# Optimization experiments

Measured on AMD Instinct MI355X. Metric: run time of the kernel, lower is better.

Reference implementation:

```python
import jax, jax.numpy as jnp
import numpy as np

N = 50000      # nodes
E = 800000     # edges (avg degree 16)
IN = 128       # in_channels
HID = 64       # hidden_channels
OUT = 64       # out_channels
H = 2          # attention heads
EDIM = 16      # edge feature dim
NEG_SLOPE = 0.2


def setup_inputs() -> dict:
    key = jax.random.key(0)
    ks = jax.random.split(key, 16)
    p = lambda k, shape: (jax.random.normal(k, shape, jnp.float32) * 0.1)
    return {
        'x': jax.random.normal(ks[0], (N, IN), jnp.float32),
        'edge_index': jax.random.randint(ks[1], (2, E), 0, N, dtype=jnp.int64),
        'edge_attr': jax.random.normal(ks[2], (E, EDIM), jnp.float32),
        # GAT layer 1 (in=IN -> HID, heads=H, concat=False, edge_dim=EDIM)
        'W1': p(ks[3], (IN, H * HID)),
        'We1': p(ks[4], (EDIM, H * HID)),
        'as1': p(ks[5], (H, HID)),
        'ad1': p(ks[6], (H, HID)),
        'ae1': p(ks[7], (H, HID)),
        'b1': jnp.zeros((HID,), jnp.float32),
        # GAT layer 2 (in=HID -> OUT)
        'W2': p(ks[8], (HID, H * OUT)),
        'We2': p(ks[9], (EDIM, H * OUT)),
        'as2': p(ks[10], (H, OUT)),
        'ad2': p(ks[11], (H, OUT)),
        'ae2': p(ks[12], (H, OUT)),
        'b2': jnp.zeros((OUT,), jnp.float32),
    }


def _add_self_loops(edge_index, edge_attr, n):
    # PyG GATConv default: add_self_loops=True, fill_value='mean' ->
    # self-loop edge_attr[i] = mean of edge_attr over edges with dst == i.
    src, dst = edge_index[0], edge_index[1]
    attr_sum = jax.ops.segment_sum(edge_attr, dst, num_segments=n)          # [N, EDIM]
    cnt = jax.ops.segment_sum(jnp.ones((edge_attr.shape[0],), edge_attr.dtype), dst, num_segments=n)
    loop_attr = attr_sum / jnp.maximum(cnt, 1.0)[:, None]
    loop = jnp.arange(n, dtype=src.dtype)
    return jnp.concatenate([src, loop]), jnp.concatenate([dst, loop]), jnp.concatenate([edge_attr, loop_attr], axis=0)


def gat_layer(x, edge_index, edge_attr, W, We, att_src, att_dst, att_edge, bias, heads, out_ch):
    """PyG GATConv with edge_dim, concat=False (mean over heads)."""
    n = x.shape[0]
    src, dst, ea = _add_self_loops(edge_index, edge_attr, n)
    h = (x @ W).reshape(n, heads, out_ch)                 # [N, H, C]
    e = (ea @ We).reshape(-1, heads, out_ch)              # [E', H, C]
    a_src = jnp.sum(h * att_src, axis=-1)                 # [N, H]
    a_dst = jnp.sum(h * att_dst, axis=-1)                 # [N, H]
    a_edge = jnp.sum(e * att_edge, axis=-1)               # [E', H]
    alpha = jax.nn.leaky_relu(a_src[src] + a_dst[dst] + a_edge, NEG_SLOPE)  # [E', H]
    # segment softmax over destination node (self-loops guarantee nonempty segments)
    amax = jax.ops.segment_max(alpha, dst, num_segments=n)
    ex = jnp.exp(alpha - amax[dst])
    denom = jax.ops.segment_sum(ex, dst, num_segments=n)
    attn = ex / (denom[dst] + 1e-16)                      # [E', H]
    msg = h[src] * attn[:, :, None]                       # [E', H, C]
    out = jax.ops.segment_sum(msg, dst, num_segments=n)   # [N, H, C]
    return jnp.mean(out, axis=1) + bias, attn


def reference(x, edge_index, edge_attr, W1, We1, as1, ad1, ae1, b1, W2, We2, as2, ad2, ae2, b2):
    h1, _attn1 = gat_layer(x, edge_index, edge_attr, W1, We1, as1, ad1, ae1, b1, H, HID)
    h1 = jax.nn.relu(h1)
    h2, _attn2 = gat_layer(h1, edge_index, edge_attr, W2, We2, as2, ad2, ae2, b2, H, OUT)
    return h2
```

## Files before the change

kernel.cpp:

```cpp
#include <hip/hip_runtime.h>

#define N_NODES 50000
#define N_EDGES 800000
#define EDIM 16
#define NEG_SLOPE 0.2f

typedef _Float16 f16x8 __attribute__((ext_vector_type(8)));
typedef _Float16 f16x2 __attribute__((ext_vector_type(2)));
typedef float f32x4 __attribute__((ext_vector_type(4)));

__global__ void count_rank_kernel(const int* __restrict__ ei, int* __restrict__ cnt,
                                  int* __restrict__ rank) {
    int e = blockIdx.x * blockDim.x + threadIdx.x;
    if (e < N_EDGES) rank[e] = atomicAdd(&cnt[ei[N_EDGES + e]], 1);
}

__global__ void scan_block_kernel(const int* __restrict__ in, int* __restrict__ excl,
                                  int* __restrict__ bsums, int n) {
    __shared__ int sh[256];
    int tid = threadIdx.x;
    int gid = blockIdx.x * 256 + tid;
    int v = (gid < n) ? in[gid] : 0;
    sh[tid] = v;
    __syncthreads();
    for (int off = 1; off < 256; off <<= 1) {
        int t = (tid >= off) ? sh[tid - off] : 0;
        __syncthreads();
        sh[tid] += t;
        __syncthreads();
    }
    if (gid < n) excl[gid] = sh[tid] - v;
    if (bsums != nullptr && tid == 255) bsums[blockIdx.x] = sh[tid];
}

__global__ void scan_add_kernel(const int* __restrict__ excl, const int* __restrict__ bs2,
                                int* __restrict__ csr_off, int n, int total) {
    int gid = blockIdx.x * 256 + threadIdx.x;
    if (gid < n) csr_off[gid] = excl[gid] + bs2[gid >> 8];
    if (gid == 0) csr_off[n] = total;
}

__global__ void we2_kernel(const float* __restrict__ We1, const float* __restrict__ ae1,
                           const float* __restrict__ We2, const float* __restrict__ ae2,
                           float* __restrict__ w_e) {
    int idx = threadIdx.x;
    if (idx >= 64) return;
    const float* We = (idx < 32) ? We1 : We2;
    const float* ae = (idx < 32) ? ae1 : ae2;
    int i = idx & 31;
    int h = i >> 4, d = i & 15;
    float s = 0.f;
    for (int c = 0; c < 64; ++c) s += We[d * 128 + h * 64 + c] * ae[h * 64 + c];
    w_e[idx] = s;
}

__global__ void scatter_pack_kernel(const int* __restrict__ ei, const float* __restrict__ edge_attr,
                                    const float* __restrict__ w_e, const int* __restrict__ csr_off,
                                    const int* __restrict__ rank, uint4* __restrict__ recs) {
    int e = blockIdx.x * blockDim.x + threadIdx.x;
    if (e >= N_EDGES) return;
    int s = ei[e];
    int d = ei[N_EDGES + e];
    const float* ea = edge_attr + (size_t)e * 16;
    float4 dd = make_float4(0.f, 0.f, 0.f, 0.f);
#pragma unroll
    for (int q = 0; q < 4; ++q) {
        float4 v = *reinterpret_cast<const float4*>(ea + q * 4);
        float4 wa = *reinterpret_cast<const float4*>(w_e + q * 4);
        float4 wb = *reinterpret_cast<const float4*>(w_e + 16 + q * 4);
        float4 wc = *reinterpret_cast<const float4*>(w_e + 32 + q * 4);
        float4 wd = *reinterpret_cast<const float4*>(w_e + 48 + q * 4);
        dd.x += v.x * wa.x + v.y * wa.y + v.z * wa.z + v.w * wa.w;
        dd.y += v.x * wb.x + v.y * wb.y + v.z * wb.z + v.w * wb.w;
        dd.z += v.x * wc.x + v.y * wc.y + v.z * wc.z + v.w * wc.w;
        dd.w += v.x * wd.x + v.y * wd.y + v.z * wd.z + v.w * wd.w;
    }
    f16x2 p1 = {(_Float16)dd.x, (_Float16)dd.y};
    f16x2 p2 = {(_Float16)dd.z, (_Float16)dd.w};
    int pos = csr_off[d] + rank[e];
    uint4 rec;
    rec.x = (unsigned)s;
    rec.y = __builtin_bit_cast(unsigned int, p1);
    rec.z = __builtin_bit_cast(unsigned int, p2);
    rec.w = 0u;
    recs[pos] = rec;
}

template <int K>
__global__ __launch_bounds__(256) void gemm_att_kernel(const float* __restrict__ X,
                                                       const float* __restrict__ W,
                                                       const float* __restrict__ as_,
                                                       const float* __restrict__ ad_,
                                                       _Float16* __restrict__ H16,
                                                       float2* __restrict__ a_src,
                                                       float2* __restrict__ a_dst, int M) {
    constexpr int NCH = K / 32;
    __shared__ _Float16 wlds[8 * NCH * 64 * 8];
    const int tid = threadIdx.x;

    for (int idx = tid; idx < K * 128; idx += 256) {
        int k = idx >> 7, c = idx & 127;
        int ct = c >> 4, cl = c & 15;
        int chunk = k >> 5, grp = (k >> 3) & 3, j = k & 7;
        wlds[(((ct * NCH) + chunk) * 64 + (grp * 16 + cl)) * 8 + j] = (_Float16)W[idx];
    }
    __syncthreads();

    const int wv = tid >> 6, lane = tid & 63;
    const int lcol = lane & 15, lgrp = lane >> 4;
    const int row0 = blockIdx.x * 64 + wv * 16;
    int arow = row0 + lcol;
    if (arow >= M) arow = M - 1;
    const float* aptr = X + (size_t)arow * K + lgrp * 8;

    f32x4 acc[8];
#pragma unroll
    for (int ct = 0; ct < 8; ++ct) acc[ct] = (f32x4){0.f, 0.f, 0.f, 0.f};

#pragma unroll
    for (int chunk = 0; chunk < NCH; ++chunk) {
        float4 va = *reinterpret_cast<const float4*>(aptr + chunk * 32);
        float4 vb = *reinterpret_cast<const float4*>(aptr + chunk * 32 + 4);
        f16x8 afrag = {(_Float16)va.x, (_Float16)va.y, (_Float16)va.z, (_Float16)va.w,
                       (_Float16)vb.x, (_Float16)vb.y, (_Float16)vb.z, (_Float16)vb.w};
#pragma unroll
        for (int ct = 0; ct < 8; ++ct) {
            f16x8 bfrag = *reinterpret_cast<const f16x8*>(&wlds[((ct * NCH + chunk) * 64 + lane) * 8]);
            acc[ct] = __builtin_amdgcn_mfma_f32_16x16x32_f16(afrag, bfrag, acc[ct], 0, 0, 0);
        }
    }

    float asv[8], adv[8];
#pragma unroll
    for (int ct = 0; ct < 8; ++ct) {
        asv[ct] = as_[ct * 16 + lcol];
        adv[ct] = ad_[ct * 16 + lcol];
    }

#pragma unroll
    for (int r = 0; r < 4; ++r) {
        int grow = row0 + lgrp * 4 + r;
        float s0 = 0.f, s1 = 0.f, d0 = 0.f, d1 = 0.f;
#pragma unroll
        for (int ct = 0; ct < 8; ++ct) {
            float v = acc[ct][r];
            if (grow < M) H16[(size_t)grow * 128 + ct * 16 + lcol] = (_Float16)v;
            if (ct < 4) { s0 += v * asv[ct]; d0 += v * adv[ct]; }
            else        { s1 += v * asv[ct]; d1 += v * adv[ct]; }
        }
#pragma unroll
        for (int m = 1; m < 16; m <<= 1) {
            s0 += __shfl_xor(s0, m);
            s1 += __shfl_xor(s1, m);
            d0 += __shfl_xor(d0, m);
            d1 += __shfl_xor(d1, m);
        }
        if (lcol == 0 && grow < M) {
            a_src[grow] = make_float2(s0, s1);
            a_dst[grow] = make_float2(d0, d1);
        }
    }
}

#define AGG_STAGE(P, TT)                                                          \
    do {                                                                          \
        float e0_ = __shfl(exv.x, (TT));                                          \
        float e1_ = __shfl(exv.y, (TT));                                          \
        float exu_ = hi ? e1_ : e0_;                                              \
        den += exu_;                                                              \
        acc0 = fmaf(exu_, (float)P.x, acc0);                                      \
        acc1 = fmaf(exu_, (float)P.y, acc1);                                      \
        int sn_ = __shfl(sv, ((TT) + 4) & 63);                                    \
        P = *reinterpret_cast<const f16x2*>(hbase + ((size_t)(unsigned)sn_ << 8)); \
    } while (0)

__global__ void aggregate_kernel(const int* __restrict__ csr_off, const uint4* __restrict__ recs,
                                 const float2* __restrict__ a_src, const float2* __restrict__ a_dst,
                                 const _Float16* __restrict__ H16, const float* __restrict__ bias,
                                 float* __restrict__ outp, int layer, int do_relu) {
    int wid = (blockIdx.x * blockDim.x + threadIdx.x) >> 6;
    int lane = threadIdx.x & 63;
    if (wid >= N_NODES) return;
    const int n = wid;
    const bool hi = lane >= 32;
    const char* hbase = reinterpret_cast<const char*>(H16) + lane * 4;

    float2 adn = a_dst[n];
    float2 asn = a_src[n];

    f16x2 hs = *reinterpret_cast<const f16x2*>(hbase + ((size_t)(unsigned)n << 8));
    float den = 0.f;
    float acc0 = 0.f;
    float acc1 = 0.f;
    float sae0 = 0.f, sae1 = 0.f;

    int b = csr_off[n], e = csr_off[n + 1];
    for (int base = b; base < e; base += 64) {
        int j = base + lane;
        bool act = j < e;
        int sv = n;
        float2 exv = make_float2(0.f, 0.f);
        if (act) {
            uint4 rec = recs[j];
            sv = (int)rec.x;
            unsigned aeu = layer ? rec.z : rec.y;
            f16x2 aev = __builtin_bit_cast(f16x2, aeu);
            float ael0 = (float)aev.x, ael1 = (float)aev.y;
            sae0 += ael0;
            sae1 += ael1;
            float2 asv = a_src[sv];
            float q0 = asv.x + adn.x + ael0;
            float q1 = asv.y + adn.y + ael1;
            q0 = (q0 > 0.f) ? q0 : NEG_SLOPE * q0;
            q1 = (q1 > 0.f) ? q1 : NEG_SLOPE * q1;
            exv = make_float2(__expf(q0), __expf(q1));
        }
        int m = e - base;
        if (m > 64) m = 64;
        int mq = (m + 3) & ~3;
        f16x2 p0, p1, p2, p3;
        int s;
        s = __shfl(sv, 0); p0 = *reinterpret_cast<const f16x2*>(hbase + ((size_t)(unsigned)s << 8));
        s = __shfl(sv, 1); p1 = *reinterpret_cast<const f16x2*>(hbase + ((size_t)(unsigned)s << 8));
        s = __shfl(sv, 2); p2 = *reinterpret_cast<const f16x2*>(hbase + ((size_t)(unsigned)s << 8));
        s = __shfl(sv, 3); p3 = *reinterpret_cast<const f16x2*>(hbase + ((size_t)(unsigned)s << 8));
        for (int t = 0; t < mq; t += 4) {
            AGG_STAGE(p0, t);
            AGG_STAGE(p1, t + 1);
            AGG_STAGE(p2, t + 2);
            AGG_STAGE(p3, t + 3);
        }
    }

#pragma unroll
    for (int m = 32; m; m >>= 1) {
        sae0 += __shfl_xor(sae0, m);
        sae1 += __shfl_xor(sae1, m);
    }
    int deg = e - b;
    float invd = (deg > 0) ? (1.f / (float)deg) : 0.f;
    float l0 = asn.x + adn.x + sae0 * invd;
    float l1 = asn.y + adn.y + sae1 * invd;
    l0 = (l0 > 0.f) ? l0 : NEG_SLOPE * l0;
    l1 = (l1 > 0.f) ? l1 : NEG_SLOPE * l1;
    float exs = hi ? __expf(l1) : __expf(l0);
    den += exs;
    acc0 = fmaf(exs, (float)hs.x, acc0);
    acc1 = fmaf(exs, (float)hs.y, acc1);

    float inv = 1.f / (den + 1e-16f);
    float r0 = acc0 * inv;
    float r1 = acc1 * inv;
    float o0 = 0.5f * (r0 + __shfl_xor(r0, 32));
    float o1 = 0.5f * (r1 + __shfl_xor(r1, 32));
    if (!hi) {
        float2 bv = *reinterpret_cast<const float2*>(bias + 2 * lane);
        o0 += bv.x;
        o1 += bv.y;
        if (do_relu) { o0 = fmaxf(o0, 0.f); o1 = fmaxf(o1, 0.f); }
        *reinterpret_cast<float2*>(outp + (size_t)n * 64 + 2 * lane) = make_float2(o0, o1);
    }
}

extern "C" void kernel_launch(void* const* d_in, const int* in_sizes, int n_in,
                              void* d_out, int out_size, void* d_ws, size_t ws_size,
                              hipStream_t stream) {
    const float* x = (const float*)d_in[0];
    const int* ei = (const int*)d_in[1];
    const float* edge_attr = (const float*)d_in[2];
    const float* W1 = (const float*)d_in[3];
    const float* We1 = (const float*)d_in[4];
    const float* as1 = (const float*)d_in[5];
    const float* ad1 = (const float*)d_in[6];
    const float* ae1 = (const float*)d_in[7];
    const float* b1 = (const float*)d_in[8];
    const float* W2 = (const float*)d_in[9];
    const float* We2 = (const float*)d_in[10];
    const float* as2 = (const float*)d_in[11];
    const float* ad2 = (const float*)d_in[12];
    const float* ae2 = (const float*)d_in[13];
    const float* b2 = (const float*)d_in[14];
    float* out = (float*)d_out;

    char* ws = (char*)d_ws;
    size_t off = 0;
    auto alloc = [&](size_t bytes) -> void* {
        void* p = ws + off;
        off += (bytes + 255) & ~(size_t)255;
        return p;
    };
    int* cnt = (int*)alloc((size_t)N_NODES * 4);
    int* csr_off = (int*)alloc(((size_t)N_NODES + 1) * 4);
    int* rank = (int*)alloc((size_t)N_EDGES * 4);
    int* excl = (int*)alloc((size_t)N_NODES * 4);
    int* bsums = (int*)alloc(256 * 4);
    int* bsums2 = (int*)alloc(256 * 4);
    uint4* recs = (uint4*)alloc((size_t)N_EDGES * 16);
    _Float16* H16 = (_Float16*)alloc((size_t)N_NODES * 128 * 2);
    float* h1 = (float*)alloc((size_t)N_NODES * 64 * 4);
    float* a_src = (float*)alloc((size_t)N_NODES * 2 * 4);
    float* a_dst = (float*)alloc((size_t)N_NODES * 2 * 4);
    float* w_e = (float*)alloc(64 * 4);

    const int nb = (N_NODES + 255) / 256;
    const int eb = (N_EDGES + 255) / 256;

    hipMemsetAsync(cnt, 0, (size_t)N_NODES * 4, stream);
    we2_kernel<<<1, 64, 0, stream>>>(We1, ae1, We2, ae2, w_e);
    count_rank_kernel<<<eb, 256, 0, stream>>>(ei, cnt, rank);
    scan_block_kernel<<<nb, 256, 0, stream>>>(cnt, excl, bsums, N_NODES);
    scan_block_kernel<<<1, 256, 0, stream>>>(bsums, bsums2, nullptr, nb);
    scan_add_kernel<<<nb, 256, 0, stream>>>(excl, bsums2, csr_off, N_NODES, N_EDGES);
    scatter_pack_kernel<<<eb, 256, 0, stream>>>(ei, edge_attr, w_e, csr_off, rank, recs);

    const int nodeWaveBlocks = (N_NODES * 64 + 255) / 256;
    const int gemmBlocks = (N_NODES + 63) / 64;

    gemm_att_kernel<128><<<gemmBlocks, 256, 0, stream>>>(x, W1, as1, ad1, H16,
                                                         (float2*)a_src, (float2*)a_dst, N_NODES);
    aggregate_kernel<<<nodeWaveBlocks, 256, 0, stream>>>(csr_off, recs,
                                                         (const float2*)a_src, (const float2*)a_dst,
                                                         H16, b1, h1, 0, 1);

    gemm_att_kernel<64><<<gemmBlocks, 256, 0, stream>>>(h1, W2, as2, ad2, H16,
                                                        (float2*)a_src, (float2*)a_dst, N_NODES);
    aggregate_kernel<<<nodeWaveBlocks, 256, 0, stream>>>(csr_off, recs,
                                                         (const float2*)a_src, (const float2*)a_dst,
                                                         H16, b2, out, 1, 0);
}
```

Baseline: 189.7 us.

## Split aggregate wave into two edge streams with 8-byte gathers; store h1 as fp16

```diff
diff --git a/kernel.cpp b/kernel.cpp
--- a/kernel.cpp
+++ b/kernel.cpp
@@ -6,6 +6,7 @@
 #define NEG_SLOPE 0.2f
 
 typedef _Float16 f16x8 __attribute__((ext_vector_type(8)));
+typedef _Float16 f16x4 __attribute__((ext_vector_type(4)));
 typedef _Float16 f16x2 __attribute__((ext_vector_type(2)));
 typedef float f32x4 __attribute__((ext_vector_type(4)));
 
@@ -86,8 +87,8 @@
     recs[pos] = rec;
 }
 
-template <int K>
-__global__ __launch_bounds__(256) void gemm_att_kernel(const float* __restrict__ X,
+template <int K, bool F16IN>
+__global__ __launch_bounds__(256) void gemm_att_kernel(const void* __restrict__ Xv,
                                                        const float* __restrict__ W,
                                                        const float* __restrict__ as_,
                                                        const float* __restrict__ ad_,
@@ -111,7 +112,6 @@
     const int row0 = blockIdx.x * 64 + wv * 16;
     int arow = row0 + lcol;
     if (arow >= M) arow = M - 1;
-    const float* aptr = X + (size_t)arow * K + lgrp * 8;
 
     f32x4 acc[8];
 #pragma unroll
@@ -119,10 +119,17 @@
 
 #pragma unroll
     for (int chunk = 0; chunk < NCH; ++chunk) {
-        float4 va = *reinterpret_cast<const float4*>(aptr + chunk * 32);
-        float4 vb = *reinterpret_cast<const float4*>(aptr + chunk * 32 + 4);
-        f16x8 afrag = {(_Float16)va.x, (_Float16)va.y, (_Float16)va.z, (_Float16)va.w,
-                       (_Float16)vb.x, (_Float16)vb.y, (_Float16)vb.z, (_Float16)vb.w};
+        f16x8 afrag;
+        if constexpr (F16IN) {
+            const _Float16* aptr = (const _Float16*)Xv + (size_t)arow * K + lgrp * 8;
+            afrag = *reinterpret_cast<const f16x8*>(aptr + chunk * 32);
+        } else {
+            const float* aptr = (const float*)Xv + (size_t)arow * K + lgrp * 8;
+            float4 va = *reinterpret_cast<const float4*>(aptr + chunk * 32);
+            float4 vb = *reinterpret_cast<const float4*>(aptr + chunk * 32 + 4);
+            afrag = (f16x8){(_Float16)va.x, (_Float16)va.y, (_Float16)va.z, (_Float16)va.w,
+                            (_Float16)vb.x, (_Float16)vb.y, (_Float16)vb.z, (_Float16)vb.w};
+        }
 #pragma unroll
         for (int ct = 0; ct < 8; ++ct) {
             f16x8 bfrag = *reinterpret_cast<const f16x8*>(&wlds[((ct * NCH + chunk) * 64 + lane) * 8]);
@@ -162,44 +169,47 @@
     }
 }
 
-#define AGG_STAGE(P, TT)                                                          \
-    do {                                                                          \
-        float e0_ = __shfl(exv.x, (TT));                                          \
-        float e1_ = __shfl(exv.y, (TT));                                          \
-        float exu_ = hi ? e1_ : e0_;                                              \
-        den += exu_;                                                              \
-        acc0 = fmaf(exu_, (float)P.x, acc0);                                      \
-        acc1 = fmaf(exu_, (float)P.y, acc1);                                      \
-        int sn_ = __shfl(sv, ((TT) + 4) & 63);                                    \
-        P = *reinterpret_cast<const f16x2*>(hbase + ((size_t)(unsigned)sn_ << 8)); \
+#define AGG_STAGE(PREG, II)                                                        \
+    do {                                                                           \
+        int sl_ = 2 * (II) + sub;                                                  \
+        float e0b_ = __shfl(ex0, sl_);                                             \
+        float e1b_ = __shfl(ex1, sl_);                                             \
+        float exu_ = h1sel ? e1b_ : e0b_;                                          \
+        int svn_ = __shfl(sv, (sl_ + 4) & 63);                                     \
+        acc0 = fmaf(exu_, (float)PREG.x, acc0);                                    \
+        acc1 = fmaf(exu_, (float)PREG.y, acc1);                                    \
+        acc2 = fmaf(exu_, (float)PREG.z, acc2);                                    \
+        acc3 = fmaf(exu_, (float)PREG.w, acc3);                                    \
+        PREG = *reinterpret_cast<const f16x4*>(hb + ((size_t)(unsigned)svn_ << 8)); \
     } while (0)
 
 __global__ void aggregate_kernel(const int* __restrict__ csr_off, const uint4* __restrict__ recs,
                                  const float2* __restrict__ a_src, const float2* __restrict__ a_dst,
                                  const _Float16* __restrict__ H16, const float* __restrict__ bias,
-                                 float* __restrict__ outp, int layer, int do_relu) {
+                                 float* __restrict__ out32, _Float16* __restrict__ out16,
+                                 int layer, int do_relu) {
     int wid = (blockIdx.x * blockDim.x + threadIdx.x) >> 6;
     int lane = threadIdx.x & 63;
     if (wid >= N_NODES) return;
     const int n = wid;
-    const bool hi = lane >= 32;
-    const char* hbase = reinterpret_cast<const char*>(H16) + lane * 4;
+    const int q = lane & 31;
+    const int sub = lane >> 5;
+    const bool h1sel = q >= 16;
+    const char* hb = reinterpret_cast<const char*>(H16) + q * 8;
 
     float2 adn = a_dst[n];
     float2 asn = a_src[n];
-
-    f16x2 hs = *reinterpret_cast<const f16x2*>(hbase + ((size_t)(unsigned)n << 8));
-    float den = 0.f;
-    float acc0 = 0.f;
-    float acc1 = 0.f;
+    int b = csr_off[n], e = csr_off[n + 1];
+
+    float acc0 = 0.f, acc1 = 0.f, acc2 = 0.f, acc3 = 0.f;
+    float den0 = 0.f, den1 = 0.f;
     float sae0 = 0.f, sae1 = 0.f;
 
-    int b = csr_off[n], e = csr_off[n + 1];
     for (int base = b; base < e; base += 64) {
         int j = base + lane;
         bool act = j < e;
         int sv = n;
-        float2 exv = make_float2(0.f, 0.f);
+        float ex0 = 0.f, ex1 = 0.f;
         if (act) {
             uint4 rec = recs[j];
             sv = (int)rec.x;
@@ -213,24 +223,36 @@
             float q1 = asv.y + adn.y + ael1;
             q0 = (q0 > 0.f) ? q0 : NEG_SLOPE * q0;
             q1 = (q1 > 0.f) ? q1 : NEG_SLOPE * q1;
-            exv = make_float2(__expf(q0), __expf(q1));
-        }
+            ex0 = __expf(q0);
+            ex1 = __expf(q1);
+        }
+        float d0 = ex0, d1 = ex1;
+#pragma unroll
+        for (int m = 32; m; m >>= 1) {
+            d0 += __shfl_xor(d0, m);
+            d1 += __shfl_xor(d1, m);
+        }
+        den0 += d0;
+        den1 += d1;
+
         int m = e - base;
         if (m > 64) m = 64;
-        int mq = (m + 3) & ~3;
-        f16x2 p0, p1, p2, p3;
-        int s;
-        s = __shfl(sv, 0); p0 = *reinterpret_cast<const f16x2*>(hbase + ((size_t)(unsigned)s << 8));
-        s = __shfl(sv, 1); p1 = *reinterpret_cast<const f16x2*>(hbase + ((size_t)(unsigned)s << 8));
-        s = __shfl(sv, 2); p2 = *reinterpret_cast<const f16x2*>(hbase + ((size_t)(unsigned)s << 8));
-        s = __shfl(sv, 3); p3 = *reinterpret_cast<const f16x2*>(hbase + ((size_t)(unsigned)s << 8));
-        for (int t = 0; t < mq; t += 4) {
-            AGG_STAGE(p0, t);
-            AGG_STAGE(p1, t + 1);
-            AGG_STAGE(p2, t + 2);
-            AGG_STAGE(p3, t + 3);
-        }
-    }
+        int nit = (m + 1) >> 1;
+        f16x4 pA, pB;
+        int s0_ = __shfl(sv, sub);
+        pA = *reinterpret_cast<const f16x4*>(hb + ((size_t)(unsigned)s0_ << 8));
+        int s1_ = __shfl(sv, 2 + sub);
+        pB = *reinterpret_cast<const f16x4*>(hb + ((size_t)(unsigned)s1_ << 8));
+        for (int i = 0; i < nit; i += 2) {
+            AGG_STAGE(pA, i);
+            AGG_STAGE(pB, i + 1);
+        }
+    }
+
+    acc0 += __shfl_xor(acc0, 32);
+    acc1 += __shfl_xor(acc1, 32);
+    acc2 += __shfl_xor(acc2, 32);
+    acc3 += __shfl_xor(acc3, 32);
 
 #pragma unroll
     for (int m = 32; m; m >>= 1) {
@@ -243,22 +265,43 @@
     float l1 = asn.y + adn.y + sae1 * invd;
     l0 = (l0 > 0.f) ? l0 : NEG_SLOPE * l0;
     l1 = (l1 > 0.f) ? l1 : NEG_SLOPE * l1;
-    float exs = hi ? __expf(l1) : __expf(l0);
-    den += exs;
-    acc0 = fmaf(exs, (float)hs.x, acc0);
-    acc1 = fmaf(exs, (float)hs.y, acc1);
-
-    float inv = 1.f / (den + 1e-16f);
-    float r0 = acc0 * inv;
-    float r1 = acc1 * inv;
-    float o0 = 0.5f * (r0 + __shfl_xor(r0, 32));
-    float o1 = 0.5f * (r1 + __shfl_xor(r1, 32));
-    if (!hi) {
-        float2 bv = *reinterpret_cast<const float2*>(bias + 2 * lane);
-        o0 += bv.x;
-        o1 += bv.y;
-        if (do_relu) { o0 = fmaxf(o0, 0.f); o1 = fmaxf(o1, 0.f); }
-        *reinterpret_cast<float2*>(outp + (size_t)n * 64 + 2 * lane) = make_float2(o0, o1);
+    float exs0 = __expf(l0), exs1 = __expf(l1);
+    den0 += exs0;
+    den1 += exs1;
+    float exsu = h1sel ? exs1 : exs0;
+    f16x4 hs = *reinterpret_cast<const f16x4*>(hb + ((size_t)(unsigned)n << 8));
+    acc0 = fmaf(exsu, (float)hs.x, acc0);
+    acc1 = fmaf(exsu, (float)hs.y, acc1);
+    acc2 = fmaf(exsu, (float)hs.z, acc2);
+    acc3 = fmaf(exsu, (float)hs.w, acc3);
+
+    float invden = 1.f / ((h1sel ? den1 : den0) + 1e-16f);
+    float r0 = acc0 * invden;
+    float r1 = acc1 * invden;
+    float r2 = acc2 * invden;
+    float r3 = acc3 * invden;
+    float t0 = __shfl_xor(r0, 16);
+    float t1 = __shfl_xor(r1, 16);
+    float t2 = __shfl_xor(r2, 16);
+    float t3 = __shfl_xor(r3, 16);
+    if (lane < 16) {
+        float4 bv = *reinterpret_cast<const float4*>(bias + q * 4);
+        float o0 = 0.5f * (r0 + t0) + bv.x;
+        float o1 = 0.5f * (r1 + t1) + bv.y;
+        float o2 = 0.5f * (r2 + t2) + bv.z;
+        float o3 = 0.5f * (r3 + t3) + bv.w;
+        if (do_relu) {
+            o0 = fmaxf(o0, 0.f); o1 = fmaxf(o1, 0.f);
+            o2 = fmaxf(o2, 0.f); o3 = fmaxf(o3, 0.f);
+        }
+        if (out32) {
+            float4 ov = {o0, o1, o2, o3};
+            *reinterpret_cast<float4*>(out32 + (size_t)n * 64 + q * 4) = ov;
+        }
+        if (out16) {
+            f16x4 ov16 = {(_Float16)o0, (_Float16)o1, (_Float16)o2, (_Float16)o3};
+            *reinterpret_cast<f16x4*>(out16 + (size_t)n * 64 + q * 4) = ov16;
+        }
     }
 }
 
@@ -297,7 +340,7 @@
     int* bsums2 = (int*)alloc(256 * 4);
     uint4* recs = (uint4*)alloc((size_t)N_EDGES * 16);
     _Float16* H16 = (_Float16*)alloc((size_t)N_NODES * 128 * 2);
-    float* h1 = (float*)alloc((size_t)N_NODES * 64 * 4);
+    _Float16* h1_16 = (_Float16*)alloc((size_t)N_NODES * 64 * 2);
     float* a_src = (float*)alloc((size_t)N_NODES * 2 * 4);
     float* a_dst = (float*)alloc((size_t)N_NODES * 2 * 4);
     float* w_e = (float*)alloc(64 * 4);
@@ -316,15 +359,15 @@
     const int nodeWaveBlocks = (N_NODES * 64 + 255) / 256;
     const int gemmBlocks = (N_NODES + 63) / 64;
 
-    gemm_att_kernel<128><<<gemmBlocks, 256, 0, stream>>>(x, W1, as1, ad1, H16,
-                                                         (float2*)a_src, (float2*)a_dst, N_NODES);
+    gemm_att_kernel<128, false><<<gemmBlocks, 256, 0, stream>>>(x, W1, as1, ad1, H16,
+                                                                (float2*)a_src, (float2*)a_dst, N_NODES);
     aggregate_kernel<<<nodeWaveBlocks, 256, 0, stream>>>(csr_off, recs,
                                                          (const float2*)a_src, (const float2*)a_dst,
-                                                         H16, b1, h1, 0, 1);
-
-    gemm_att_kernel<64><<<gemmBlocks, 256, 0, stream>>>(h1, W2, as2, ad2, H16,
-                                                        (float2*)a_src, (float2*)a_dst, N_NODES);
+                                                         H16, b1, nullptr, h1_16, 0, 1);
+
+    gemm_att_kernel<64, true><<<gemmBlocks, 256, 0, stream>>>(h1_16, W2, as2, ad2, H16,
+                                                              (float2*)a_src, (float2*)a_dst, N_NODES);
     aggregate_kernel<<<nodeWaveBlocks, 256, 0, stream>>>(csr_off, recs,
                                                          (const float2*)a_src, (const float2*)a_dst,
-                                                         H16, b2, out, 1, 0);
-}
+                                                         H16, b2, out, nullptr, 1, 0);
+}
```

After: 188.3 us. About the same (-0.7%).
